# Optimization experiments

Measured on AMD Instinct MI355X. Metric: run time of the kernel, lower is better.

Reference implementation:

```python
import jax, jax.numpy as jnp
import numpy as np

ALPHA = 0.2  # leakyrelu negative slope
NEG_INF = -1.0e12


def setup_inputs() -> dict:
    key = jax.random.key(0)
    k1, k2, k3, k4, k5 = jax.random.split(key, 5)
    B, N, C_in, C_out = 8, 2048, 256, 256
    inp = jax.random.normal(k1, (B, N, C_in), dtype=jnp.float32)
    adj = jax.random.randint(k2, (N, N), 0, 2, dtype=jnp.int32)
    # xavier_uniform with gain=1.414 for (C_in, C_out)
    limit = 1.414 * np.sqrt(6.0 / (C_in + C_out))
    W1 = jax.random.uniform(k3, (C_in, C_out), jnp.float32, -limit, limit)
    W2 = jax.random.uniform(k4, (C_in, C_out), jnp.float32, -limit, limit)
    W3 = jax.random.uniform(k5, (C_in, C_out), jnp.float32, -limit, limit)
    return {"inp": inp, "adj": adj, "W1": W1, "W2": W2, "W3": W3}


def reference(inp, adj, W1, W2, W3):
    # inp: [B,N,Cin], adj: [N,N], W*: [Cin,Cout]
    h1 = jnp.einsum('bnc,cd->bnd', inp, W1)  # [B,N,Cout] queries
    h2 = jnp.einsum('bnc,cd->bnd', inp, W2)  # [B,N,Cout] keys
    h3 = jnp.einsum('bnc,cd->bnd', inp, W3)  # [B,N,Cout] values
    e = jnp.einsum('bnd,bmd->bnm', h1, h2)   # [B,N,N] scores
    e = jax.nn.leaky_relu(e, ALPHA)
    e = jnp.where(adj[None, :, :] > 0, e, NEG_INF)
    attention = jax.nn.softmax(e, axis=-1)   # dropout p=0 / eval mode -> identity
    h_prime = jnp.einsum('bnm,bmd->bnd', attention, h3)
    return jax.nn.relu(h_prime)  # concat=True
```

## Files before the change

kernel.cpp:

```cpp
#include <hip/hip_runtime.h>

typedef __bf16 bf16_t;
typedef __bf16 bf16x4 __attribute__((ext_vector_type(4)));
typedef __bf16 bf16x8 __attribute__((ext_vector_type(8)));
typedef float floatx4 __attribute__((ext_vector_type(4)));
typedef signed char i8_t;
typedef int intx4 __attribute__((ext_vector_type(4)));

__device__ inline void split_hl(float v, bf16_t& hi, bf16_t& lo) {
    hi = (bf16_t)v;
    lo = (bf16_t)(v - (float)hi);
}

__global__ void adjbits_kernel(const int* __restrict__ adj, unsigned* __restrict__ bits) {
    int id = blockIdx.x * 256 + threadIdx.x;
    const int* p = adj + (size_t)id * 32;
    unsigned w = 0;
#pragma unroll
    for (int j = 0; j < 32; j += 4) {
        int4 v = *(const int4*)(p + j);
        w |= (v.x > 0 ? 1u : 0u) << j;
        w |= (v.y > 0 ? 1u : 0u) << (j + 1);
        w |= (v.z > 0 ? 1u : 0u) << (j + 2);
        w |= (v.w > 0 ? 1u : 0u) << (j + 3);
    }
    bits[id] = w;
}

__global__ void wtrans_kernel(const float* __restrict__ W1,
                              const float* __restrict__ W2,
                              const float* __restrict__ W3,
                              bf16_t* __restrict__ Wthi, bf16_t* __restrict__ Wtlo) {
    __shared__ float T[64 * 68];
    const int zi = blockIdx.z;
    const float* W = (zi == 0) ? W1 : ((zi == 1) ? W2 : W3);
    bf16_t* ohi = Wthi + zi * 256 * 256;
    bf16_t* olo = Wtlo + zi * 256 * 256;
    const int c0 = blockIdx.x * 64, d0 = blockIdx.y * 64;
    const int tid = threadIdx.x;
#pragma unroll
    for (int i = 0; i < 4; i++) {
        int idx = i * 256 + tid;
        int r = idx >> 4, c4 = (idx & 15) * 4;
        floatx4 v = *(const floatx4*)(W + (c0 + r) * 256 + d0 + c4);
        *(floatx4*)(&T[r * 68 + c4]) = v;
    }
    __syncthreads();
#pragma unroll
    for (int i = 0; i < 4; i++) {
        int idx = i * 256 + tid;
        int rd = idx & 63, cc4 = (idx >> 6) * 4;
        bf16x4 vh, vl;
#pragma unroll
        for (int ii = 0; ii < 4; ii++) {
            float v = T[(cc4 + ii) * 68 + rd];
            bf16_t h, l; split_hl(v, h, l);
            vh[ii] = h; vl[ii] = l;
        }
        *(bf16x4*)(ohi + (d0 + rd) * 256 + c0 + cc4) = vh;
        *(bf16x4*)(olo + (d0 + rd) * 256 + c0 + cc4) = vl;
    }
}

__global__ __launch_bounds__(256) void proj_kernel(
    const float* __restrict__ X,
    const bf16_t* __restrict__ Wthi, const bf16_t* __restrict__ Wtlo,
    i8_t* __restrict__ Q8h, i8_t* __restrict__ Q8l, float* __restrict__ sqv,
    i8_t* __restrict__ K8h, i8_t* __restrict__ K8l, float* __restrict__ skv,
    bf16_t* __restrict__ H3t) {
    __shared__ bf16_t Xh[64 * 40], Xl[64 * 40];
    __shared__ bf16_t Wh[256 * 40], Wl[256 * 40];
    const int z = blockIdx.y;
    const int row0 = blockIdx.x * 64;
    const int tid = threadIdx.x;
    const int w = tid >> 6, lane = tid & 63;
    const int m = lane & 15, q = lane >> 4;
    const bf16_t* Wzh = Wthi + z * 256 * 256;
    const bf16_t* Wzl = Wtlo + z * 256 * 256;

    floatx4 acc[16];
#pragma unroll
    for (int i = 0; i < 16; i++) acc[i] = (floatx4){0.f, 0.f, 0.f, 0.f};

    for (int c0 = 0; c0 < 256; c0 += 32) {
#pragma unroll
        for (int i = 0; i < 2; i++) {
            int idx = i * 256 + tid;
            int r = idx >> 3, c4 = (idx & 7) * 4;
            floatx4 v = *(const floatx4*)(X + (size_t)(row0 + r) * 256 + c0 + c4);
            bf16x4 vh, vl;
#pragma unroll
            for (int ii = 0; ii < 4; ii++) {
                bf16_t h, l; split_hl(v[ii], h, l);
                vh[ii] = h; vl[ii] = l;
            }
            *(bf16x4*)(&Xh[r * 40 + c4]) = vh;
            *(bf16x4*)(&Xl[r * 40 + c4]) = vl;
        }
#pragma unroll
        for (int i = 0; i < 4; i++) {
            int idx = i * 256 + tid;
            int d = idx >> 2, c8 = (idx & 3) * 8;
            *(bf16x8*)(&Wh[d * 40 + c8]) = *(const bf16x8*)(Wzh + d * 256 + c0 + c8);
            *(bf16x8*)(&Wl[d * 40 + c8]) = *(const bf16x8*)(Wzl + d * 256 + c0 + c8);
        }
        __syncthreads();
        bf16x8 ah = *(const bf16x8*)(&Xh[(w * 16 + m) * 40 + q * 8]);
        bf16x8 al = *(const bf16x8*)(&Xl[(w * 16 + m) * 40 + q * 8]);
#pragma unroll
        for (int nt = 0; nt < 16; nt++) {
            bf16x8 bh = *(const bf16x8*)(&Wh[(nt * 16 + m) * 40 + q * 8]);
            bf16x8 bl = *(const bf16x8*)(&Wl[(nt * 16 + m) * 40 + q * 8]);
            acc[nt] = __builtin_amdgcn_mfma_f32_16x16x32_bf16(ah, bh, acc[nt], 0, 0, 0);
            acc[nt] = __builtin_amdgcn_mfma_f32_16x16x32_bf16(ah, bl, acc[nt], 0, 0, 0);
            acc[nt] = __builtin_amdgcn_mfma_f32_16x16x32_bf16(al, bh, acc[nt], 0, 0, 0);
        }
        __syncthreads();
    }
    const int rbase = row0 + w * 16 + q * 4;
    if (z < 2) {
        i8_t* Dh = (z == 0) ? Q8h : K8h;
        i8_t* Dl = (z == 0) ? Q8l : K8l;
        float* sv = (z == 0) ? sqv : skv;
        float am[4] = {0.f, 0.f, 0.f, 0.f};
#pragma unroll
        for (int nt = 0; nt < 16; nt++)
#pragma unroll
            for (int r = 0; r < 4; r++) am[r] = fmaxf(am[r], fabsf(acc[nt][r]));
#pragma unroll
        for (int off = 1; off < 16; off <<= 1)
#pragma unroll
            for (int r = 0; r < 4; r++)
                am[r] = fmaxf(am[r], __shfl_xor(am[r], off, 64));
        float sc[4], inv[4];
#pragma unroll
        for (int r = 0; r < 4; r++) {
            sc[r]  = (am[r] > 0.f) ? am[r] * (1.f / 127.f) : 1.f;
            inv[r] = (am[r] > 0.f) ? 127.f / am[r] : 0.f;
        }
#pragma unroll
        for (int nt = 0; nt < 16; nt++)
#pragma unroll
            for (int r = 0; r < 4; r++) {
                float vq = acc[nt][r] * inv[r];
                float qh = rintf(vq);
                float ql = fminf(fmaxf(rintf((vq - qh) * 256.f), -127.f), 127.f);
                int offo = (rbase + r) * 256 + nt * 16 + m;
                Dh[offo] = (i8_t)(int)qh;
                Dl[offo] = (i8_t)(int)ql;
            }
        if (m == 0) {
#pragma unroll
            for (int r = 0; r < 4; r++) sv[rbase + r] = sc[r];
        }
    } else {
#pragma unroll
        for (int nt = 0; nt < 16; nt++)
#pragma unroll
            for (int r = 0; r < 4; r++) {
                int token = rbase + r;
                int b = token >> 11, n = token & 2047;
                H3t[(size_t)(b * 256 + nt * 16 + m) * 2048 + n] = (bf16_t)acc[nt][r];
            }
    }
}

#define K8SW(row, off) ((off) ^ (((row) & 7) << 4))
#define VSW(row, off)  ((off) ^ ((((row) >> 1) & 3) << 4))
__global__ __launch_bounds__(256, 2) void attn_kernel(
    const i8_t* __restrict__ Q8h, const i8_t* __restrict__ Q8l,
    const float* __restrict__ sqv,
    const i8_t* __restrict__ K8h, const i8_t* __restrict__ K8l,
    const float* __restrict__ skv,
    const bf16_t* __restrict__ H3t, const unsigned* __restrict__ adjbits,
    bf16_t* __restrict__ Opart, float* __restrict__ mpart, float* __restrict__ lpart,
    int klen) {
    __shared__ i8_t K8[2][32 * 256];
    __shared__ bf16_t Vl[256 * 32];
    __shared__ bf16_t Pl[4][16 * 32];

    const int nwg = (int)(gridDim.x * gridDim.y * gridDim.z);
    const int wgid = (int)(blockIdx.x + (blockIdx.y << 5) + (blockIdx.z << 8));
    const int nid = (wgid & 7) * (nwg >> 3) + (wgid >> 3);
    const int qb = nid & 31;
    const int b  = (nid >> 5) & 7;
    const int kz = nid >> 8;

    const int q0 = qb * 64;
    const int tid = threadIdx.x;
    const int w = tid >> 6, lane = tid & 63;
    const int m = lane & 15, q = lane >> 4;

    char* K8B0 = (char*)&K8[0][0];
    char* K8B1 = (char*)&K8[1][0];
    char* VlB  = (char*)&Vl[0];
    char* PlB  = (char*)&Pl[w][0];

    const i8_t* qrh = Q8h + (size_t)(b * 2048 + q0 + w * 16 + m) * 256;
    const i8_t* qrl = Q8l + (size_t)(b * 2048 + q0 + w * 16 + m) * 256;
    intx4 qh8[4], ql8[4];
#pragma unroll
    for (int ck = 0; ck < 4; ck++) {
        qh8[ck] = *(const intx4*)(qrh + ck * 64 + q * 16);
        ql8[ck] = *(const intx4*)(qrl + ck * 64 + q * 16);
    }
    float sq4[4];
#pragma unroll
    for (int r = 0; r < 4; r++) sq4[r] = sqv[b * 2048 + q0 + w * 16 + q * 4 + r];

    bf16x8 vones;
#pragma unroll
    for (int i = 0; i < 8; i++) vones[i] = (bf16_t)1.0f;

    float m_run[4];
#pragma unroll
    for (int r = 0; r < 4; r++) m_run[r] = -3.0e38f;
    floatx4 l_acc = (floatx4){0.f, 0.f, 0.f, 0.f};
    floatx4 o[16];
#pragma unroll
    for (int i = 0; i < 16; i++) o[i] = (floatx4){0.f, 0.f, 0.f, 0.f};

    const unsigned* bitrow[4];
#pragma unroll
    for (int r = 0; r < 4; r++)
        bitrow[r] = adjbits + (size_t)(q0 + w * 16 + q * 4 + r) * 64;

    intx4 rkh[2], rkl[2];
    bf16x8 rvv[4];
    float skt[2], skn[2];
    const int kbeg = kz * klen, kend = kbeg + klen;

#pragma unroll
    for (int i = 0; i < 2; i++) {
        int ci = i * 256 + tid;
        int kr = ci >> 4, cb = (ci & 15) * 16;
        rkh[i] = *(const intx4*)(K8h + (size_t)(b * 2048 + kbeg + kr) * 256 + cb);
        rkl[i] = *(const intx4*)(K8l + (size_t)(b * 2048 + kbeg + kr) * 256 + cb);
    }
#pragma unroll
    for (int i = 0; i < 4; i++) {
        int ci = i * 256 + tid;
        int d = ci >> 2, k8 = (ci & 3) * 8;
        rvv[i] = *(const bf16x8*)(H3t + (size_t)(b * 256 + d) * 2048 + kbeg + k8);
    }
    skt[0] = skv[b * 2048 + kbeg + m];
    skt[1] = skv[b * 2048 + kbeg + 16 + m];

    for (int k0 = kbeg; k0 < kend; k0 += 32) {
        __syncthreads();
#pragma unroll
        for (int i = 0; i < 2; i++) {
            int ci = i * 256 + tid;
            int kr = ci >> 4, cb = (ci & 15) * 16;
            *(intx4*)(K8B0 + K8SW(kr, kr * 256 + cb)) = rkh[i];
            *(intx4*)(K8B1 + K8SW(kr, kr * 256 + cb)) = rkl[i];
        }
#pragma unroll
        for (int i = 0; i < 4; i++) {
            int ci = i * 256 + tid;
            int d = ci >> 2, kb = (ci & 3) * 16;
            *(bf16x8*)(VlB + VSW(d, d * 64 + kb)) = rvv[i];
        }
        __syncthreads();
        if (k0 + 32 < kend) {
            int kn = k0 + 32;
#pragma unroll
            for (int i = 0; i < 2; i++) {
                int ci = i * 256 + tid;
                int kr = ci >> 4, cb = (ci & 15) * 16;
                rkh[i] = *(const intx4*)(K8h + (size_t)(b * 2048 + kn + kr) * 256 + cb);
                rkl[i] = *(const intx4*)(K8l + (size_t)(b * 2048 + kn + kr) * 256 + cb);
            }
#pragma unroll
            for (int i = 0; i < 4; i++) {
                int ci = i * 256 + tid;
                int d = ci >> 2, k8 = (ci & 3) * 8;
                rvv[i] = *(const bf16x8*)(H3t + (size_t)(b * 256 + d) * 2048 + kn + k8);
            }
            skn[0] = skv[b * 2048 + kn + m];
            skn[1] = skv[b * 2048 + kn + 16 + m];
        }

        float s[2][4];
#pragma unroll
        for (int t = 0; t < 2; t++) {
            intx4 ch = {0, 0, 0, 0}, cm = {0, 0, 0, 0};
            const int row = t * 16 + m;
#pragma unroll
            for (int ck = 0; ck < 4; ck++) {
                const int cb2 = ck * 64 + q * 16;
                intx4 kh = *(const intx4*)(K8B0 + K8SW(row, row * 256 + cb2));
                intx4 kl = *(const intx4*)(K8B1 + K8SW(row, row * 256 + cb2));
                ch = __builtin_amdgcn_mfma_i32_16x16x64_i8(qh8[ck], kh, ch, 0, 0, 0);
                cm = __builtin_amdgcn_mfma_i32_16x16x64_i8(qh8[ck], kl, cm, 0, 0, 0);
                cm = __builtin_amdgcn_mfma_i32_16x16x64_i8(ql8[ck], kh, cm, 0, 0, 0);
            }
#pragma unroll
            for (int r = 0; r < 4; r++)
                s[t][r] = fmaf((float)cm[r], 0.00390625f, (float)ch[r]) * (sq4[r] * skt[t]);
        }

        unsigned aw[4];
#pragma unroll
        for (int r = 0; r < 4; r++) aw[r] = bitrow[r][k0 >> 5];
        float p[2][4], tmax[4];
#pragma unroll
        for (int r = 0; r < 4; r++) tmax[r] = -3.0e38f;
#pragma unroll
        for (int t = 0; t < 2; t++)
#pragma unroll
            for (int r = 0; r < 4; r++) {
                float v = s[t][r];
                v = (v > 0.f) ? v : 0.2f * v;
                v = ((aw[r] >> (t * 16 + m)) & 1u) ? v : -1.0e12f;
                p[t][r] = v;
                tmax[r] = fmaxf(tmax[r], v);
            }
#pragma unroll
        for (int off = 1; off < 16; off <<= 1)
#pragma unroll
            for (int r = 0; r < 4; r++)
                tmax[r] = fmaxf(tmax[r], __shfl_xor(tmax[r], off, 64));

        int rise = 0;
        float mnew[4];
#pragma unroll
        for (int r = 0; r < 4; r++) {
            mnew[r] = fmaxf(m_run[r], tmax[r]);
            rise |= (mnew[r] > m_run[r]);
        }
        if (__any(rise)) {
#pragma unroll
            for (int r = 0; r < 4; r++) {
                float alpha = __expf(m_run[r] - mnew[r]);
                m_run[r] = mnew[r];
                l_acc[r] *= alpha;
#pragma unroll
                for (int nt = 0; nt < 16; nt++) o[nt][r] *= alpha;
            }
        }
#pragma unroll
        for (int t = 0; t < 2; t++)
#pragma unroll
            for (int r = 0; r < 4; r++)
                p[t][r] = __expf(p[t][r] - m_run[r]);

#pragma unroll
        for (int t = 0; t < 2; t++)
#pragma unroll
            for (int r = 0; r < 4; r++) {
                int row = q * 4 + r;
                *(bf16_t*)(PlB + VSW(row, row * 64 + (t * 16 + m) * 2)) = (bf16_t)p[t][r];
            }
        bf16x8 pf = *(const bf16x8*)(PlB + VSW(m, m * 64 + q * 16));

        l_acc = __builtin_amdgcn_mfma_f32_16x16x32_bf16(pf, vones, l_acc, 0, 0, 0);

#pragma unroll
        for (int nt = 0; nt < 16; nt++) {
            const int vr = nt * 16 + m;
            bf16x8 vf = *(const bf16x8*)(VlB + VSW(vr, vr * 64 + q * 16));
            o[nt] = __builtin_amdgcn_mfma_f32_16x16x32_bf16(pf, vf, o[nt], 0, 0, 0);
        }
        skt[0] = skn[0];
        skt[1] = skn[1];
    }

    const int rowg = kz * 16384 + b * 2048 + q0 + w * 16 + q * 4;
#pragma unroll
    for (int nt = 0; nt < 16; nt++)
#pragma unroll
        for (int r = 0; r < 4; r++)
            Opart[(size_t)(rowg + r) * 256 + nt * 16 + m] = (bf16_t)o[nt][r];
    if (m == 0) {
#pragma unroll
        for (int r = 0; r < 4; r++) {
            mpart[rowg + r] = m_run[r];
            lpart[rowg + r] = l_acc[r];
        }
    }
}

__global__ __launch_bounds__(256) void merge_kernel(
    const bf16_t* __restrict__ Opart, const float* __restrict__ mpart,
    const float* __restrict__ lpart, float* __restrict__ out, int S) {
    int gid = blockIdx.x * 256 + threadIdx.x;
    int row = gid >> 6, c4 = (gid & 63) * 4;
    float M = -3.0e38f;
    for (int s = 0; s < S; s++) M = fmaxf(M, mpart[s * 16384 + row]);
    float denom = 0.f;
    float4 acc = make_float4(0.f, 0.f, 0.f, 0.f);
    for (int s = 0; s < S; s++) {
        float sc = __expf(mpart[s * 16384 + row] - M);
        denom += lpart[s * 16384 + row] * sc;
        bf16x4 v = *(const bf16x4*)(Opart + ((size_t)(s * 16384 + row)) * 256 + c4);
        acc.x += (float)v[0] * sc; acc.y += (float)v[1] * sc;
        acc.z += (float)v[2] * sc; acc.w += (float)v[3] * sc;
    }
    float inv = 1.f / denom;
    float4 r;
    r.x = fmaxf(acc.x * inv, 0.f);
    r.y = fmaxf(acc.y * inv, 0.f);
    r.z = fmaxf(acc.z * inv, 0.f);
    r.w = fmaxf(acc.w * inv, 0.f);
    *(float4*)(out + (size_t)row * 256 + c4) = r;
}

extern "C" void kernel_launch(void* const* d_in, const int* in_sizes, int n_in,
                              void* d_out, int out_size, void* d_ws, size_t ws_size,
                              hipStream_t stream) {
    const float* X   = (const float*)d_in[0];
    const int*   adj = (const int*)d_in[1];
    const float* W1  = (const float*)d_in[2];
    const float* W2  = (const float*)d_in[3];
    const float* W3  = (const float*)d_in[4];
    float* out = (float*)d_out;

    char* ws = (char*)d_ws;
    i8_t* Q8h = (i8_t*)(ws + ((size_t)0 << 20));
    i8_t* Q8l = (i8_t*)(ws + ((size_t)4 << 20));
    i8_t* K8h = (i8_t*)(ws + ((size_t)8 << 20));
    i8_t* K8l = (i8_t*)(ws + ((size_t)12 << 20));
    bf16_t* H3t = (bf16_t*)(ws + ((size_t)16 << 20));
    float* sqv = (float*)(ws + ((size_t)24 << 20));
    float* skv = (float*)(ws + ((size_t)24 << 20) + 65536);
    size_t wt0 = ((size_t)24 << 20) + 131072;
    bf16_t* Wthi = (bf16_t*)(ws + wt0);
    bf16_t* Wtlo = (bf16_t*)(ws + wt0 + 393216);
    float* mpart = (float*)(ws + wt0);
    float* lpart = (float*)(ws + wt0 + 131072);
    unsigned* adjb = (unsigned*)(ws + wt0 + 786432);
    size_t opart_off = wt0 + 786432 + 524288;
    const size_t need2 = opart_off + (size_t)2 * 16384 * 256 * 2;

    int S = (ws_size >= need2) ? 2 : 1;
    bf16_t* Opart = (bf16_t*)(ws + opart_off);

    adjbits_kernel<<<512, 256, 0, stream>>>(adj, adjb);
    wtrans_kernel<<<dim3(4, 4, 3), 256, 0, stream>>>(W1, W2, W3, Wthi, Wtlo);
    proj_kernel<<<dim3(256, 3), 256, 0, stream>>>(X, Wthi, Wtlo,
                                                  Q8h, Q8l, sqv, K8h, K8l, skv, H3t);
    attn_kernel<<<dim3(32, 8, S), 256, 0, stream>>>(Q8h, Q8l, sqv, K8h, K8l, skv,
                                                    H3t, adjb, Opart, mpart, lpart,
                                                    2048 / S);
    merge_kernel<<<4096, 256, 0, stream>>>(Opart, mpart, lpart, out, S);
}
```

Measured before the change: 235.6 us.

## Fuse adjacency bitpacking into projection kernel and retile waves to 32x128

Adjacency bit-packing runs as extra blocks inside the projection kernel, removing a separate launch and letting both workloads overlap on the GPU. The projection waves switch from 16 rows x 256 columns to 32 rows x 128 columns, so each W fragment loaded from LDS feeds two MFMA row tiles. Because a row's output columns are now split across two waves, the per-row int8 quantization max is combined through shared memory with an added barrier.

```diff
diff --git a/kernel.cpp b/kernel.cpp
--- a/kernel.cpp
+++ b/kernel.cpp
@@ -10,21 +10,6 @@
 __device__ inline void split_hl(float v, bf16_t& hi, bf16_t& lo) {
     hi = (bf16_t)v;
     lo = (bf16_t)(v - (float)hi);
-}
-
-__global__ void adjbits_kernel(const int* __restrict__ adj, unsigned* __restrict__ bits) {
-    int id = blockIdx.x * 256 + threadIdx.x;
-    const int* p = adj + (size_t)id * 32;
-    unsigned w = 0;
-#pragma unroll
-    for (int j = 0; j < 32; j += 4) {
-        int4 v = *(const int4*)(p + j);
-        w |= (v.x > 0 ? 1u : 0u) << j;
-        w |= (v.y > 0 ? 1u : 0u) << (j + 1);
-        w |= (v.z > 0 ? 1u : 0u) << (j + 2);
-        w |= (v.w > 0 ? 1u : 0u) << (j + 3);
-    }
-    bits[id] = w;
 }
 
 __global__ void wtrans_kernel(const float* __restrict__ W1,
@@ -62,19 +47,41 @@
     }
 }
 
-__global__ __launch_bounds__(256) void proj_kernel(
+__global__ __launch_bounds__(256) void projadj_kernel(
     const float* __restrict__ X,
     const bf16_t* __restrict__ Wthi, const bf16_t* __restrict__ Wtlo,
     i8_t* __restrict__ Q8h, i8_t* __restrict__ Q8l, float* __restrict__ sqv,
     i8_t* __restrict__ K8h, i8_t* __restrict__ K8l, float* __restrict__ skv,
-    bf16_t* __restrict__ H3t) {
+    bf16_t* __restrict__ H3t,
+    const int* __restrict__ adj, unsigned* __restrict__ bits) {
     __shared__ bf16_t Xh[64 * 40], Xl[64 * 40];
     __shared__ bf16_t Wh[256 * 40], Wl[256 * 40];
-    const int z = blockIdx.y;
-    const int row0 = blockIdx.x * 64;
+    __shared__ float amS[2][64];
+
     const int tid = threadIdx.x;
+    const int blk = blockIdx.x;
+    if (blk < 512) {
+        int id = blk * 256 + tid;
+        const int* p = adj + (size_t)id * 32;
+        unsigned wbits = 0;
+#pragma unroll
+        for (int j = 0; j < 32; j += 4) {
+            int4 v = *(const int4*)(p + j);
+            wbits |= (v.x > 0 ? 1u : 0u) << j;
+            wbits |= (v.y > 0 ? 1u : 0u) << (j + 1);
+            wbits |= (v.z > 0 ? 1u : 0u) << (j + 2);
+            wbits |= (v.w > 0 ? 1u : 0u) << (j + 3);
+        }
+        bits[id] = wbits;
+        return;
+    }
+
+    const int pblk = blk - 512;
+    const int z = pblk >> 8;
+    const int row0 = (pblk & 255) * 64;
     const int w = tid >> 6, lane = tid & 63;
     const int m = lane & 15, q = lane >> 4;
+    const int wr = w >> 1, wc = w & 1;
     const bf16_t* Wzh = Wthi + z * 256 * 256;
     const bf16_t* Wzl = Wtlo + z * 256 * 256;
 
@@ -105,63 +112,100 @@
             *(bf16x8*)(&Wl[d * 40 + c8]) = *(const bf16x8*)(Wzl + d * 256 + c0 + c8);
         }
         __syncthreads();
-        bf16x8 ah = *(const bf16x8*)(&Xh[(w * 16 + m) * 40 + q * 8]);
-        bf16x8 al = *(const bf16x8*)(&Xl[(w * 16 + m) * 40 + q * 8]);
-#pragma unroll
-        for (int nt = 0; nt < 16; nt++) {
-            bf16x8 bh = *(const bf16x8*)(&Wh[(nt * 16 + m) * 40 + q * 8]);
-            bf16x8 bl = *(const bf16x8*)(&Wl[(nt * 16 + m) * 40 + q * 8]);
-            acc[nt] = __builtin_amdgcn_mfma_f32_16x16x32_bf16(ah, bh, acc[nt], 0, 0, 0);
-            acc[nt] = __builtin_amdgcn_mfma_f32_16x16x32_bf16(ah, bl, acc[nt], 0, 0, 0);
-            acc[nt] = __builtin_amdgcn_mfma_f32_16x16x32_bf16(al, bh, acc[nt], 0, 0, 0);
+        bf16x8 ah[2], al[2];
+#pragma unroll
+        for (int rt = 0; rt < 2; rt++) {
+            ah[rt] = *(const bf16x8*)(&Xh[(wr * 32 + rt * 16 + m) * 40 + q * 8]);
+            al[rt] = *(const bf16x8*)(&Xl[(wr * 32 + rt * 16 + m) * 40 + q * 8]);
+        }
+#pragma unroll
+        for (int ct = 0; ct < 8; ct++) {
+            bf16x8 bh = *(const bf16x8*)(&Wh[(wc * 128 + ct * 16 + m) * 40 + q * 8]);
+            bf16x8 bl = *(const bf16x8*)(&Wl[(wc * 128 + ct * 16 + m) * 40 + q * 8]);
+#pragma unroll
+            for (int rt = 0; rt < 2; rt++) {
+                acc[rt * 8 + ct] = __builtin_amdgcn_mfma_f32_16x16x32_bf16(ah[rt], bh, acc[rt * 8 + ct], 0, 0, 0);
+                acc[rt * 8 + ct] = __builtin_amdgcn_mfma_f32_16x16x32_bf16(ah[rt], bl, acc[rt * 8 + ct], 0, 0, 0);
+                acc[rt * 8 + ct] = __builtin_amdgcn_mfma_f32_16x16x32_bf16(al[rt], bh, acc[rt * 8 + ct], 0, 0, 0);
+            }
         }
         __syncthreads();
     }
-    const int rbase = row0 + w * 16 + q * 4;
+
     if (z < 2) {
         i8_t* Dh = (z == 0) ? Q8h : K8h;
         i8_t* Dl = (z == 0) ? Q8l : K8l;
         float* sv = (z == 0) ? sqv : skv;
-        float am[4] = {0.f, 0.f, 0.f, 0.f};
-#pragma unroll
-        for (int nt = 0; nt < 16; nt++)
-#pragma unroll
-            for (int r = 0; r < 4; r++) am[r] = fmaxf(am[r], fabsf(acc[nt][r]));
+        float am[2][4];
+#pragma unroll
+        for (int rt = 0; rt < 2; rt++)
+#pragma unroll
+            for (int r = 0; r < 4; r++) am[rt][r] = 0.f;
+#pragma unroll
+        for (int ct = 0; ct < 8; ct++)
+#pragma unroll
+            for (int rt = 0; rt < 2; rt++)
+#pragma unroll
+                for (int r = 0; r < 4; r++)
+                    am[rt][r] = fmaxf(am[rt][r], fabsf(acc[rt * 8 + ct][r]));
 #pragma unroll
         for (int off = 1; off < 16; off <<= 1)
 #pragma unroll
-            for (int r = 0; r < 4; r++)
-                am[r] = fmaxf(am[r], __shfl_xor(am[r], off, 64));
-        float sc[4], inv[4];
-#pragma unroll
-        for (int r = 0; r < 4; r++) {
-            sc[r]  = (am[r] > 0.f) ? am[r] * (1.f / 127.f) : 1.f;
-            inv[r] = (am[r] > 0.f) ? 127.f / am[r] : 0.f;
-        }
-#pragma unroll
-        for (int nt = 0; nt < 16; nt++)
+            for (int rt = 0; rt < 2; rt++)
+#pragma unroll
+                for (int r = 0; r < 4; r++)
+                    am[rt][r] = fmaxf(am[rt][r], __shfl_xor(am[rt][r], off, 64));
+        if (m == 0) {
+#pragma unroll
+            for (int rt = 0; rt < 2; rt++)
+#pragma unroll
+                for (int r = 0; r < 4; r++)
+                    amS[wc][wr * 32 + rt * 16 + q * 4 + r] = am[rt][r];
+        }
+        __syncthreads();
+        float sc[2][4], inv[2][4];
+#pragma unroll
+        for (int rt = 0; rt < 2; rt++)
 #pragma unroll
             for (int r = 0; r < 4; r++) {
-                float vq = acc[nt][r] * inv[r];
-                float qh = rintf(vq);
-                float ql = fminf(fmaxf(rintf((vq - qh) * 256.f), -127.f), 127.f);
-                int offo = (rbase + r) * 256 + nt * 16 + m;
-                Dh[offo] = (i8_t)(int)qh;
-                Dl[offo] = (i8_t)(int)ql;
-            }
-        if (m == 0) {
-#pragma unroll
-            for (int r = 0; r < 4; r++) sv[rbase + r] = sc[r];
+                int row = wr * 32 + rt * 16 + q * 4 + r;
+                float a = fmaxf(amS[0][row], amS[1][row]);
+                sc[rt][r]  = (a > 0.f) ? a * (1.f / 127.f) : 1.f;
+                inv[rt][r] = (a > 0.f) ? 127.f / a : 0.f;
+            }
+#pragma unroll
+        for (int ct = 0; ct < 8; ct++)
+#pragma unroll
+            for (int rt = 0; rt < 2; rt++)
+#pragma unroll
+                for (int r = 0; r < 4; r++) {
+                    float vq = acc[rt * 8 + ct][r] * inv[rt][r];
+                    float qh = rintf(vq);
+                    float ql = fminf(fmaxf(rintf((vq - qh) * 256.f), -127.f), 127.f);
+                    int offo = (row0 + wr * 32 + rt * 16 + q * 4 + r) * 256 +
+                               wc * 128 + ct * 16 + m;
+                    Dh[offo] = (i8_t)(int)qh;
+                    Dl[offo] = (i8_t)(int)ql;
+                }
+        if (m == 0 && wc == 0) {
+#pragma unroll
+            for (int rt = 0; rt < 2; rt++)
+#pragma unroll
+                for (int r = 0; r < 4; r++)
+                    sv[row0 + wr * 32 + rt * 16 + q * 4 + r] = sc[rt][r];
         }
     } else {
 #pragma unroll
-        for (int nt = 0; nt < 16; nt++)
-#pragma unroll
-            for (int r = 0; r < 4; r++) {
-                int token = rbase + r;
-                int b = token >> 11, n = token & 2047;
-                H3t[(size_t)(b * 256 + nt * 16 + m) * 2048 + n] = (bf16_t)acc[nt][r];
-            }
+        for (int ct = 0; ct < 8; ct++)
+#pragma unroll
+            for (int rt = 0; rt < 2; rt++)
+#pragma unroll
+                for (int r = 0; r < 4; r++) {
+                    int token = row0 + wr * 32 + rt * 16 + q * 4 + r;
+                    int b = token >> 11, n = token & 2047;
+                    H3t[(size_t)(b * 256 + wc * 128 + ct * 16 + m) * 2048 + n] =
+                        (bf16_t)acc[rt * 8 + ct][r];
+                }
     }
 }
 
@@ -436,10 +480,10 @@
     int S = (ws_size >= need2) ? 2 : 1;
     bf16_t* Opart = (bf16_t*)(ws + opart_off);
 
-    adjbits_kernel<<<512, 256, 0, stream>>>(adj, adjb);
     wtrans_kernel<<<dim3(4, 4, 3), 256, 0, stream>>>(W1, W2, W3, Wthi, Wtlo);
-    proj_kernel<<<dim3(256, 3), 256, 0, stream>>>(X, Wthi, Wtlo,
-                                                  Q8h, Q8l, sqv, K8h, K8l, skv, H3t);
+    projadj_kernel<<<1280, 256, 0, stream>>>(X, Wthi, Wtlo,
+                                             Q8h, Q8l, sqv, K8h, K8l, skv, H3t,
+                                             adj, adjb);
     attn_kernel<<<dim3(32, 8, S), 256, 0, stream>>>(Q8h, Q8l, sqv, K8h, K8l, skv,
                                                     H3t, adjb, Opart, mpart, lpart,
                                                     2048 / S);
```

Result: faster. 218.4 us (-7.3%).
